# Performance work log

Hardware: AMD Instinct MI355X
Metric: run time of the kernel (lower is better)

Reference implementation:

```python
import jax, jax.numpy as jnp
import numpy as np
import math

B, C, H, W = 128, 128, 16, 16
E, NH, MEM, K = 128, 8, 8, 3
HD = E // NH            # head dim = 16
D = H * W * E // NH     # tot_head_dim = 4096
ATTN_MASK_B = 3.0
EPS = 1e-5


def conv_same(x, w, b):
    # x: (B, Cin, H, W), w: (Cout, Cin, K, K)  -- matches torch Conv2d with padding=K//2
    y = jax.lax.conv_general_dilated(x, w, (1, 1), 'SAME',
                                     dimension_numbers=('NCHW', 'OIHW', 'NCHW'))
    return y + b[None, :, None, None]


def setup_inputs() -> dict:
    key = jax.random.key(0)
    ks = jax.random.split(key, 12)
    s = 0.02
    return {
        'input':    jax.random.normal(ks[0], (B, C, H, W), jnp.float32),
        'h_cur':    jax.random.normal(ks[1], (B, E, H, W), jnp.float32),
        'c_cur':    jax.random.normal(ks[2], (B, E, H, W), jnp.float32),
        'concat_k': jax.random.normal(ks[3], (B, NH, MEM, D), jnp.float32),
        'concat_v': jax.random.normal(ks[4], (B, NH, MEM, D), jnp.float32),
        'attn_mask': jax.random.bernoulli(ks[5], 0.3, (B * NH, 1, MEM)),
        'main_w':   jax.random.normal(ks[6], (5 * E, C + E, K, K), jnp.float32) * s,
        'main_b':   jnp.zeros((5 * E,), jnp.float32),
        'proj_w':   jax.random.normal(ks[7], (3 * E, C, K, K), jnp.float32) * s,
        'proj_b':   jnp.zeros((3 * E,), jnp.float32),
        'out_w':    jax.random.normal(ks[8], (E, E, K, K), jnp.float32) * s,
        'out_b':    jnp.zeros((E,), jnp.float32),
        'norm_w':   jnp.ones((E, H, W), jnp.float32),
        'norm_b':   jnp.zeros((E, H, W), jnp.float32),
        'pos_w':    jax.random.normal(ks[9], (MEM, H * W * E), jnp.float32) * s,
        'pos_b':    jax.random.uniform(ks[10], (MEM, NH), jnp.float32, -0.1, 0.1),
    }


def reference(input, h_cur, c_cur, concat_k, concat_v, attn_mask,
              main_w, main_b, proj_w, proj_b, out_w, out_b,
              norm_w, norm_b, pos_w, pos_b):
    b = input.shape[0]
    BH = b * NH

    # ---- ConvLSTM gates (5 * embed_dim channels) ----
    combined = jnp.concatenate([input, h_cur], axis=1)           # (B, C+E, H, W)
    cc = conv_same(combined, main_w, main_b)                     # (B, 5E, H, W)
    cc_i, cc_f, cc_o, cc_g, cc_a = jnp.split(cc, 5, axis=1)
    i = jax.nn.sigmoid(cc_i)
    f = jax.nn.sigmoid(cc_f)
    o = jax.nn.sigmoid(cc_o)
    g = jnp.tanh(cc_g)
    a = jax.nn.sigmoid(cc_a)
    c_next = f * c_cur + i * g

    # ---- attention over rolling memory ----
    kqv = conv_same(input, proj_w, proj_b)                       # (B, 3E, H, W)
    kqv = kqv.reshape(BH, 3 * HD, H * W)                         # per-head groups of 3*HD channels
    k_new, q, v_new = jnp.split(kqv, 3, axis=1)                  # each (BH, HD, HW)
    flat = lambda x: x.reshape(BH, 1, D)                         # (BH, 1, tot_head_dim)
    q = flat(q) / math.sqrt(D)
    k_new, v_new = flat(k_new), flat(v_new)

    # slide memory: drop oldest slot, append new k/v
    k = jnp.concatenate([concat_k.reshape(BH, MEM, D)[:, 1:], k_new], axis=1)  # (BH, MEM, D)
    v = jnp.concatenate([concat_v.reshape(BH, MEM, D)[:, 1:], v_new], axis=1)

    # learned positional terms: pos_w added to keys, pos_b added to scores
    pw = pos_w.reshape(MEM, NH, D).transpose(1, 0, 2)            # (NH, MEM, D)
    k = (k.reshape(b, NH, MEM, D) + pw[None]).reshape(BH, MEM, D)
    pb = jnp.broadcast_to(pos_b.T[None], (b, NH, MEM)).reshape(BH, 1, MEM)

    # custom mask: -inf where masked, then last (newest) slot forced to +attn_mask_b bias
    mask_f = jnp.where(attn_mask, -jnp.inf, 0.0).astype(q.dtype)
    mask_f = mask_f.at[:, :, -1].set(ATTN_MASK_B)                # (BH, 1, MEM)

    scores = mask_f + jnp.einsum('bqd,bmd->bqm', q, k) + pb      # (BH, 1, MEM)
    attn_weights = jax.nn.softmax(scores, axis=-1)
    attn_out = jnp.einsum('bqm,bmd->bqd', attn_weights, v)       # (BH, 1, D)
    attn_out = attn_out.reshape(b, E, H, W)                      # (b,NH,HD,H,W)->(b,E,H,W)

    out = conv_same(attn_out, out_w, out_b) + input[:, :E]
    # LayerNorm over (E, H, W)
    mu = jnp.mean(out, axis=(1, 2, 3), keepdims=True)
    var = jnp.mean(jnp.square(out - mu), axis=(1, 2, 3), keepdims=True)
    out = (out - mu) * jax.lax.rsqrt(var + EPS) * norm_w[None] + norm_b[None]

    c_next = c_next + a * jnp.tanh(out)
    h_next = o * jnp.tanh(c_next)

    ret_k = k.reshape(b, NH, MEM, D)
    ret_v = v.reshape(b, NH, MEM, D)
    return h_next, c_next, ret_k, ret_v
```

## Files before the change

kernel.cpp:

```cpp
#include <hip/hip_runtime.h>
#include <hip/hip_bf16.h>

typedef __hip_bfloat16 bf16;
typedef __attribute__((ext_vector_type(8))) short bf16x8;
typedef __attribute__((ext_vector_type(4))) float f32x4;

__device__ __forceinline__ float b2f(bf16 x){ return __bfloat162float(x); }
__device__ __forceinline__ bf16  f2b(float x){ return __float2bfloat16(x); }
__device__ __forceinline__ float sigm(float x){ return 1.f/(1.f+__expf(-x)); }

__device__ __forceinline__ int sniff_bf16(const void* nw){
    return ((const unsigned short*)nw)[0] != 0;
}
__device__ __forceinline__ float ldf(const void* p, size_t i, int isb){
    return isb ? b2f(((const bf16*)p)[i]) : ((const float*)p)[i];
}
__device__ __forceinline__ void stf(void* p, size_t i, float v, int isb){
    if (isb) ((bf16*)p)[i] = f2b(v);
    else     ((float*)p)[i] = v;
}
__device__ __forceinline__ void ld8(const void* p, size_t i, int isb, float* a){
    if (isb){
        union{ uint4 u; bf16 h[8]; } x;
        x.u = *(const uint4*)((const bf16*)p + i);
        #pragma unroll
        for (int q=0;q<8;q++) a[q] = b2f(x.h[q]);
    } else {
        const float4* f4 = (const float4*)((const float*)p + i);
        float4 v0 = f4[0], v1 = f4[1];
        a[0]=v0.x;a[1]=v0.y;a[2]=v0.z;a[3]=v0.w;
        a[4]=v1.x;a[5]=v1.y;a[6]=v1.z;a[7]=v1.w;
    }
}
__device__ __forceinline__ void st8(void* p, size_t i, const float* a, int isb){
    if (isb){
        union{ uint4 u; bf16 h[8]; } o;
        #pragma unroll
        for (int q=0;q<8;q++) o.h[q] = f2b(a[q]);
        *(uint4*)((bf16*)p + i) = o.u;
    } else {
        float4* f4 = (float4*)((float*)p + i);
        f4[0] = make_float4(a[0],a[1],a[2],a[3]);
        f4[1] = make_float4(a[4],a[5],a[6],a[7]);
    }
}

#define H_OFF  0u
#define C_OFF  4194304u
#define RK_OFF 8388608u
#define RV_OFF 41943040u

__global__ void k_rearrange_mfma(const void* __restrict__ w, bf16* __restrict__ wrB,
                                 int nst, int NT, int mode,
                                 const void* __restrict__ nw)
{
    int isb = sniff_bf16(nw);
    int tid = blockIdx.x*256 + threadIdx.x;
    int total = nst*36*NT*64;
    if (tid >= total) return;
    int lane = tid & 63; int r = tid >> 6;
    int nt = r % NT; int kc = r / NT;
    int cb = kc & 3; int tp = (kc>>2) % 9; int s = kc / 36;
    int n = lane & 15, lg = lane >> 4;
    int oc;
    if (mode == 1){ int eb = nt/5, g = nt%5; oc = g*128 + eb*16 + n; }
    else if (mode == 2){ int h = nt/3, rr = nt%3; oc = h*48 + rr*16 + n; }
    else oc = nt*16 + n;
    int Cin = nst*128;
    int ci0 = s*128 + cb*32 + lg*8;
    size_t base = ((size_t)oc*Cin + ci0)*9 + tp;
    bf16* o = wrB + (size_t)tid*8;
    #pragma unroll
    for (int j=0;j<8;j++) o[j] = f2b(ldf(w, base + (size_t)j*9, isb));
}

__device__ __forceinline__ void stage_img(bf16* lds, const void* src, size_t base,
                                          int t, int isb)
{
    if (isb){
        const uint4* s4 = (const uint4*)((const bf16*)src + base);
        uint4* l4 = (uint4*)lds;
        for (int i=t; i<4096; i+=256) l4[i] = s4[i];
    } else {
        const float4* s4 = (const float4*)((const float*)src + base);
        for (int i=t; i<8192; i+=256){
            float4 v = s4[i];
            int j = i*4;
            lds[j]=f2b(v.x); lds[j+1]=f2b(v.y); lds[j+2]=f2b(v.z); lds[j+3]=f2b(v.w);
        }
    }
}

__global__ __launch_bounds__(256,2) void k_transpose(const void* __restrict__ src,
                                                     bf16* __restrict__ dst,
                                                     int nst, int sidx,
                                                     const void* __restrict__ nwp)
{
    int isb = nwp ? sniff_bf16(nwp) : 1;
    int b = blockIdx.x, t = threadIdx.x;
    __shared__ bf16 lds[32768];
    stage_img(lds, src, (size_t)b*32768, t, isb);
    __syncthreads();
    char* dimg = (char*)(dst + ((size_t)b*nst + sidx)*32768);
    int swz = (t & 7) << 4;
    for (int cb=0; cb<16; ++cb){
        union { uint4 u; bf16 h[8]; } o;
        #pragma unroll
        for (int q=0;q<8;q++) o.h[q] = lds[(cb*8+q)*256 + t];
        *(uint4*)(dimg + t*256 + ((cb*16) ^ swz)) = o.u;
    }
}

template<int NF, int NST>
__device__ __forceinline__ void conv_mfma(const bf16* __restrict__ xTimg,
                                          const bf16* __restrict__ wrB,
                                          int ntbase, int NT,
                                          bf16* lds, f32x4 (&acc)[4][NF])
{
    const int t = threadIdx.x;
    const int wid = t >> 6, lane = t & 63;
    const int lg = lane >> 4, x = lane & 15;
    union U { uint4 u; bf16x8 v; };

    for (int s=0; s<NST; ++s){
        __syncthreads();
        {
            const uint4* g4 = (const uint4*)(xTimg + (size_t)s*32768);
            uint4* l4 = (uint4*)lds;
            #pragma unroll
            for (int i=0;i<16;++i) l4[t + i*256] = g4[t + i*256];
        }
        __syncthreads();
        for (int tap=0; tap<9; ++tap){
            const int dy = tap/3 - 1, dx = tap%3 - 1;
            const int xx = x + dx;
            const bool xok = (unsigned)xx < 16u;
            const int xc = xx & 15;
            const int swz = (xc & 7) << 4;
            const char* ldsb = (const char*)lds;
            #pragma unroll
            for (int cb=0; cb<4; ++cb){
                U B[NF];
                const bf16* wb = wrB + ((size_t)(((s*9 + tap)*4 + cb)*NT + ntbase)*64 + lane)*8;
                #pragma unroll
                for (int nf=0; nf<NF; ++nf) B[nf].u = *(const uint4*)(wb + nf*512);
                const int cofs = (cb*64 + lg*16) ^ swz;
                #pragma unroll
                for (int mt=0; mt<4; ++mt){
                    const int yy = wid*4 + mt + dy;
                    if ((unsigned)yy < 16u){
                        U A;
                        A.u = *(const uint4*)(ldsb + (yy*16 + xc)*256 + cofs);
                        if (!xok) A.u = make_uint4(0u,0u,0u,0u);
                        #pragma unroll
                        for (int nf=0; nf<NF; ++nf)
                            acc[mt][nf] = __builtin_amdgcn_mfma_f32_16x16x32_bf16(
                                              A.v, B[nf].v, acc[mt][nf], 0, 0, 0);
                    }
                }
            }
        }
    }
}

template<int NF, int NFI>
__device__ __forceinline__ void epi_stage(float* lf, const f32x4 (&acc)[4][NF],
                                          int slotrow, int wid, int lg, int e)
{
    #pragma unroll
    for (int mt=0; mt<4; ++mt){
        int p = wid*64 + mt*16 + lg*4;
        #pragma unroll
        for (int r=0; r<4; ++r)
            lf[(slotrow + e)*257 + p + r] = acc[mt][NFI][r];
    }
}

__global__ __launch_bounds__(256,2) void k_main_mfma(
    const bf16* __restrict__ xT, const bf16* __restrict__ wrB,
    const void* __restrict__ bias, const void* __restrict__ ccur,
    bf16* __restrict__ wc, bf16* __restrict__ wo, bf16* __restrict__ wa,
    const void* __restrict__ nwp)
{
    int isb = sniff_bf16(nwp);
    int b = blockIdx.x, ocb = blockIdx.y, t = threadIdx.x;
    __shared__ bf16 lds[32768];
    f32x4 acc[4][5];
    const f32x4 z4 = {0.f,0.f,0.f,0.f};
    #pragma unroll
    for (int mt=0;mt<4;++mt)
        #pragma unroll
        for (int nf=0;nf<5;++nf) acc[mt][nf] = z4;

    conv_mfma<5,2>(xT + (size_t)b*65536, wrB, ocb*5, 40, lds, acc);

    __syncthreads();
    float* lf = (float*)lds;
    int wid = t>>6, lane = t&63, lg = lane>>4, e = lane&15;
    epi_stage<5,0>(lf, acc, 0,  wid, lg, e);
    epi_stage<5,1>(lf, acc, 16, wid, lg, e);
    epi_stage<5,3>(lf, acc, 32, wid, lg, e);
    __syncthreads();
    #pragma unroll
    for (int j=0;j<16;++j){
        int eg = ocb*16 + j;
        float gi = sigm (lf[(     j)*257 + t] + ldf(bias,       eg, isb));
        float gf = sigm (lf[(16 + j)*257 + t] + ldf(bias, 128 + eg, isb));
        float gg = tanhf(lf[(32 + j)*257 + t] + ldf(bias, 384 + eg, isb));
        size_t idx = ((size_t)b*128 + eg)*256 + t;
        float cp = ldf(ccur, idx, isb);
        wc[idx] = f2b(gf*cp + gi*gg);
    }
    __syncthreads();
    epi_stage<5,2>(lf, acc, 0,  wid, lg, e);
    epi_stage<5,4>(lf, acc, 16, wid, lg, e);
    __syncthreads();
    #pragma unroll
    for (int j=0;j<16;++j){
        int eg = ocb*16 + j;
        size_t idx = ((size_t)b*128 + eg)*256 + t;
        wo[idx] = f2b(sigm(lf[(     j)*257 + t] + ldf(bias, 256 + eg, isb)));
        wa[idx] = f2b(sigm(lf[(16 + j)*257 + t] + ldf(bias, 512 + eg, isb)));
    }
}

__global__ __launch_bounds__(256,2) void k_proj_mfma(
    const bf16* __restrict__ xT, const bf16* __restrict__ wrB,
    const void* __restrict__ bias, const void* __restrict__ pos_w,
    void* dout, bf16* __restrict__ wq, const void* __restrict__ nwp)
{
    int isb = sniff_bf16(nwp);
    int b = blockIdx.x, h = blockIdx.y, t = threadIdx.x;
    __shared__ bf16 lds[32768];
    f32x4 acc[4][3];
    const f32x4 z4 = {0.f,0.f,0.f,0.f};
    #pragma unroll
    for (int mt=0;mt<4;++mt)
        #pragma unroll
        for (int nf=0;nf<3;++nf) acc[mt][nf] = z4;

    conv_mfma<3,1>(xT + (size_t)b*65536, wrB, h*3, 24, lds, acc);

    __syncthreads();
    float* lf = (float*)lds;
    int wid = t>>6, lane = t&63, lg = lane>>4, e = lane&15;
    epi_stage<3,0>(lf, acc, 0,  wid, lg, e);
    epi_stage<3,1>(lf, acc, 16, wid, lg, e);
    epi_stage<3,2>(lf, acc, 32, wid, lg, e);
    __syncthreads();
    int bh = b*8 + h;
    #pragma unroll
    for (int j=0;j<16;++j){
        float kv = lf[(     j)*257 + t] + ldf(bias, h*48 +      j, isb);
        float qv = lf[(16 + j)*257 + t] + ldf(bias, h*48 + 16 + j, isb);
        float vv = lf[(32 + j)*257 + t] + ldf(bias, h*48 + 32 + j, isb);
        int d = j*256 + t;
        size_t kd = ((size_t)bh*8 + 7)*4096 + d;
        stf(dout, RK_OFF + kd, kv + ldf(pos_w, (size_t)7*32768 + h*4096 + d, isb), isb);
        stf(dout, RV_OFF + kd, vv, isb);
        wq[(size_t)bh*4096 + d] = f2b(qv * 0.015625f);
    }
}

__global__ __launch_bounds__(256,2) void k_out_mfma(
    const bf16* __restrict__ attnT, const bf16* __restrict__ wrB,
    const void* __restrict__ bias, const void* __restrict__ xin,
    bf16* __restrict__ wln, const void* __restrict__ nwp)
{
    int isb = sniff_bf16(nwp);
    int b = blockIdx.x, ocb = blockIdx.y, t = threadIdx.x;
    __shared__ bf16 lds[32768];
    f32x4 acc[4][2];
    const f32x4 z4 = {0.f,0.f,0.f,0.f};
    #pragma unroll
    for (int mt=0;mt<4;++mt)
        #pragma unroll
        for (int nf=0;nf<2;++nf) acc[mt][nf] = z4;

    conv_mfma<2,1>(attnT + (size_t)b*32768, wrB, ocb*2, 8, lds, acc);

    __syncthreads();
    float* lf = (float*)lds;
    int wid = t>>6, lane = t&63, lg = lane>>4, e = lane&15;
    epi_stage<2,0>(lf, acc, 0,  wid, lg, e);
    epi_stage<2,1>(lf, acc, 16, wid, lg, e);
    __syncthreads();
    #pragma unroll
    for (int o=0;o<32;++o){
        int oc = ocb*32 + o;
        size_t idx = ((size_t)b*128 + oc)*256 + t;
        wln[idx] = f2b(lf[o*257 + t] + ldf(bias, oc, isb) + ldf(xin, idx, isb));
    }
}

__global__ __launch_bounds__(256,2) void k_slide_attn(
    const void* __restrict__ ck, const void* __restrict__ cv,
    const void* __restrict__ pos_w, const bf16* __restrict__ wq,
    const int* __restrict__ mask, const void* __restrict__ pos_b,
    void* dout, bf16* __restrict__ attnT, const void* __restrict__ nwp)
{
    int isb = sniff_bf16(nwp);
    int bh = blockIdx.x, t = threadIdx.x;
    int b = bh >> 3, h = bh & 7;
    __shared__ float sbuf[4096];

    float qreg[2][8];
    #pragma unroll
    for (int j=0;j<2;j++){
        union{ uint4 u; bf16 hh[8]; } x;
        x.u = *(const uint4*)(wq + (size_t)bh*4096 + (size_t)(j*256+t)*8);
        #pragma unroll
        for (int q=0;q<8;q++) qreg[j][q] = b2f(x.hh[q]);
    }

    float part[8];
    #pragma unroll
    for (int m=0;m<8;m++) part[m]=0.f;
    for (int m=0;m<8;m++){
        #pragma unroll
        for (int j=0;j<2;j++){
            size_t d0 = (size_t)(j*256+t)*8;
            float a[8];
            if (m < 7){
                ld8(ck, ((size_t)bh*8 + m + 1)*4096 + d0, isb, a);
                float pv[8];
                ld8(pos_w, (size_t)m*32768 + (size_t)h*4096 + d0, isb, pv);
                #pragma unroll
                for (int q=0;q<8;q++) a[q] += pv[q];
                st8(dout, RK_OFF + ((size_t)bh*8 + m)*4096 + d0, a, isb);
            } else {
                ld8(dout, RK_OFF + ((size_t)bh*8 + 7)*4096 + d0, isb, a);
            }
            #pragma unroll
            for (int q=0;q<8;q++) part[m] = fmaf(qreg[j][q], a[q], part[m]);
        }
    }
    #pragma unroll
    for (int m=0;m<8;m++) sbuf[m*256 + t] = part[m];
    __syncthreads();
    for (int s=128; s>0; s>>=1){
        if (t < s){
            #pragma unroll
            for (int m=0;m<8;m++) sbuf[m*256 + t] += sbuf[m*256 + t + s];
        }
        __syncthreads();
    }
    float w[8]; float mx = -1e30f;
    #pragma unroll
    for (int m=0;m<8;m++){
        float mf = (m==7) ? 3.0f : (mask[bh*8+m] ? -INFINITY : 0.0f);
        w[m] = mf + sbuf[m*256] + ldf(pos_b, m*8 + h, isb);
        mx = fmaxf(mx, w[m]);
    }
    float ssum = 0.f;
    #pragma unroll
    for (int m=0;m<8;m++){ w[m] = __expf(w[m]-mx); ssum += w[m]; }
    float inv = 1.f/ssum;
    #pragma unroll
    for (int m=0;m<8;m++) w[m] *= inv;
    __syncthreads();

    float acc[2][8];
    #pragma unroll
    for (int j=0;j<2;j++)
        #pragma unroll
        for (int q=0;q<8;q++) acc[j][q]=0.f;
    for (int m=0;m<8;m++){
        #pragma unroll
        for (int j=0;j<2;j++){
            size_t d0 = (size_t)(j*256+t)*8;
            float a[8];
            if (m < 7){
                ld8(cv, ((size_t)bh*8 + m + 1)*4096 + d0, isb, a);
                st8(dout, RV_OFF + ((size_t)bh*8 + m)*4096 + d0, a, isb);
            } else {
                ld8(dout, RV_OFF + ((size_t)bh*8 + 7)*4096 + d0, isb, a);
            }
            #pragma unroll
            for (int q=0;q<8;q++) acc[j][q] = fmaf(w[m], a[q], acc[j][q]);
        }
    }
    #pragma unroll
    for (int j=0;j<2;j++){
        int chl = j*8 + (t>>5);
        int base = chl*256 + (t&31)*8;
        *(float4*)&sbuf[base    ] = make_float4(acc[j][0],acc[j][1],acc[j][2],acc[j][3]);
        *(float4*)&sbuf[base + 4] = make_float4(acc[j][4],acc[j][5],acc[j][6],acc[j][7]);
    }
    __syncthreads();
    int px = t, swz = (px & 7) << 4;
    union{ uint4 u; bf16 hh[8]; } o0, o1;
    #pragma unroll
    for (int jj=0;jj<8;jj++){
        o0.hh[jj] = f2b(sbuf[ jj     *256 + px]);
        o1.hh[jj] = f2b(sbuf[(jj+8)  *256 + px]);
    }
    char* dimg = (char*)(attnT + (size_t)b*32768);
    *(uint4*)(dimg + px*256 + ((h*32     ) ^ swz)) = o0.u;
    *(uint4*)(dimg + px*256 + ((h*32 + 16) ^ swz)) = o1.u;
}

__global__ __launch_bounds__(1024,1) void k_ln_stats(
    const bf16* __restrict__ wln, float2* __restrict__ stats)
{
    int b = blockIdx.x, t = threadIdx.x;
    float s = 0.f, s2 = 0.f;
    #pragma unroll
    for (int i=0;i<4;i++){
        union{ uint4 u; bf16 hh[8]; } x;
        x.u = *(const uint4*)(wln + (size_t)b*32768 + (size_t)(i*1024+t)*8);
        #pragma unroll
        for (int q=0;q<8;q++){ float v = b2f(x.hh[q]); s += v; s2 += v*v; }
    }
    #pragma unroll
    for (int off=32; off>0; off>>=1){
        s  += __shfl_down(s,  off);
        s2 += __shfl_down(s2, off);
    }
    __shared__ float r1[16], r2[16];
    int wv = t >> 6;
    if ((t & 63) == 0){ r1[wv] = s; r2[wv] = s2; }
    __syncthreads();
    if (t == 0){
        float a = 0.f, c = 0.f;
        #pragma unroll
        for (int k=0;k<16;k++){ a += r1[k]; c += r2[k]; }
        float mean = a * (1.f/32768.f);
        float var  = c * (1.f/32768.f) - mean*mean;
        stats[b] = make_float2(mean, rsqrtf(var + 1e-5f));
    }
}

__global__ __launch_bounds__(256,2) void k_ln_apply(
    const bf16* __restrict__ wln, const bf16* __restrict__ wc,
    const bf16* __restrict__ wo,  const bf16* __restrict__ wa,
    const void* __restrict__ nw,  const void* __restrict__ nb,
    const float2* __restrict__ stats, void* dout)
{
    int isb = sniff_bf16(nw);
    int b = blockIdx.x, sg = blockIdx.y, t = threadIdx.x;
    float2 mv = stats[b];
    float mean = mv.x, rs = mv.y;
    #pragma unroll
    for (int j=0;j<2;j++){
        size_t i  = (size_t)sg*4096 + (size_t)(j*256+t)*8;
        size_t gi = (size_t)b*32768 + i;
        union{ uint4 u; bf16 hh[8]; } xl, xc, xo, xa;
        xl.u = *(const uint4*)(wln + gi);
        xc.u = *(const uint4*)(wc  + gi);
        xo.u = *(const uint4*)(wo  + gi);
        xa.u = *(const uint4*)(wa  + gi);
        float nwv[8], nbv[8];
        ld8(nw, i, isb, nwv);
        ld8(nb, i, isb, nbv);
        float cts[8], hs[8];
        #pragma unroll
        for (int q=0;q<8;q++){
            float xln = (b2f(xl.hh[q]) - mean)*rs*nwv[q] + nbv[q];
            float ct  = b2f(xc.hh[q]) + b2f(xa.hh[q])*tanhf(xln);
            cts[q] = ct;
            hs[q]  = b2f(xo.hh[q])*tanhf(ct);
        }
        st8(dout, C_OFF + gi, cts, isb);
        st8(dout, H_OFF + gi, hs,  isb);
    }
}

extern "C" void kernel_launch(void* const* d_in, const int* in_sizes, int n_in,
                              void* d_out, int out_size, void* d_ws, size_t ws_size,
                              hipStream_t stream)
{
    const void* xin  = d_in[0];
    const void* hcur = d_in[1];
    const void* ccur = d_in[2];
    const void* ck   = d_in[3];
    const void* cv   = d_in[4];
    const int*  mask = (const int*) d_in[5];
    const void* mw   = d_in[6];
    const void* mb   = d_in[7];
    const void* pw   = d_in[8];
    const void* pb   = d_in[9];
    const void* ow   = d_in[10];
    const void* ob   = d_in[11];
    const void* nw   = d_in[12];
    const void* nb   = d_in[13];
    const void* posw = d_in[14];
    const void* posb = d_in[15];

    char* ws = (char*)d_ws;
    bf16* wrB_main = (bf16*)(ws + 0);
    bf16* wrB_proj = (bf16*)(ws + 2949120);
    bf16* wrB_out  = (bf16*)(ws + 3833856);
    bf16* wc  = (bf16*)(ws + 4128768);
    bf16* wo  = (bf16*)(ws + 12517376);
    bf16* wa  = (bf16*)(ws + 20905984);
    bf16* wq  = (bf16*)(ws + 29294592);
    bf16* wln = wq;
    float2* lnstats = (float2*)(ws + 37683200);

    bf16* xT    = (bf16*)d_out;
    bf16* attnT = xT + 4194304;

    k_rearrange_mfma<<<720,256,0,stream>>>(mw, wrB_main, 2, 40, 1, nw);
    k_rearrange_mfma<<<216,256,0,stream>>>(pw, wrB_proj, 1, 24, 2, nw);
    k_rearrange_mfma<<< 72,256,0,stream>>>(ow, wrB_out,  1,  8, 0, nw);

    k_transpose<<<128,256,0,stream>>>(xin,  xT, 2, 0, nw);
    k_transpose<<<128,256,0,stream>>>(hcur, xT, 2, 1, nw);

    k_main_mfma <<<dim3(128,8),256,0,stream>>>(xT, wrB_main, mb, ccur, wc, wo, wa, nw);
    k_proj_mfma <<<dim3(128,8),256,0,stream>>>(xT, wrB_proj, pb, posw, d_out, wq, nw);
    k_slide_attn<<<1024,       256,0,stream>>>(ck, cv, posw, wq, mask, posb, d_out, attnT, nw);
    k_out_mfma  <<<dim3(128,4),256,0,stream>>>(attnT, wrB_out, ob, xin, wln, nw);
    k_ln_stats  <<<128,       1024,0,stream>>>(wln, lnstats);
    k_ln_apply  <<<dim3(128,8),256,0,stream>>>(wln, wc, wo, wa, nw, nb, lnstats, d_out);
}
```

Measured before the change: 831.0 us.

## Halve conv LDS staging, fuse LN stats into out conv, merge transposes

The conv helper now stages each input image in two channel halves (128-byte rows), which shrinks the LDS footprint. Launch bounds are raised so more blocks fit per CU. LayerNorm statistics are accumulated in the output-conv epilogue with atomics, which removes the separate stats kernel but needs a memset to zero them first. The two transpose launches become one 2D grid, and the attention score reduction uses wave shuffles instead of an LDS tree. The trade-off is extra syncs per half-stage, a possible register-pressure increase, and non-deterministic atomic ordering in the stats.

```diff
diff --git a/kernel.cpp b/kernel.cpp
--- a/kernel.cpp
+++ b/kernel.cpp
@@ -91,22 +91,23 @@
     }
 }
 
-__global__ __launch_bounds__(256,2) void k_transpose(const void* __restrict__ src,
-                                                     bf16* __restrict__ dst,
-                                                     int nst, int sidx,
-                                                     const void* __restrict__ nwp)
-{
-    int isb = nwp ? sniff_bf16(nwp) : 1;
-    int b = blockIdx.x, t = threadIdx.x;
+__global__ __launch_bounds__(256,2) void k_transpose2(const void* __restrict__ x,
+                                                      const void* __restrict__ h,
+                                                      bf16* __restrict__ dst,
+                                                      const void* __restrict__ nwp)
+{
+    int isb = sniff_bf16(nwp);
+    int b = blockIdx.x, sidx = blockIdx.y, t = threadIdx.x;
+    const void* src = sidx ? h : x;
     __shared__ bf16 lds[32768];
     stage_img(lds, src, (size_t)b*32768, t, isb);
     __syncthreads();
-    char* dimg = (char*)(dst + ((size_t)b*nst + sidx)*32768);
+    char* dimg = (char*)(dst + ((size_t)b*2 + sidx)*32768);
     int swz = (t & 7) << 4;
     for (int cb=0; cb<16; ++cb){
-        union { uint4 u; bf16 h[8]; } o;
-        #pragma unroll
-        for (int q=0;q<8;q++) o.h[q] = lds[(cb*8+q)*256 + t];
+        union { uint4 u; bf16 hh[8]; } o;
+        #pragma unroll
+        for (int q=0;q<8;q++) o.hh[q] = lds[(cb*8+q)*256 + t];
         *(uint4*)(dimg + t*256 + ((cb*16) ^ swz)) = o.u;
     }
 }
@@ -120,42 +121,49 @@
     const int t = threadIdx.x;
     const int wid = t >> 6, lane = t & 63;
     const int lg = lane >> 4, x = lane & 15;
+    const int q8 = t & 7, pxg = t >> 3;
     union U { uint4 u; bf16x8 v; };
 
     for (int s=0; s<NST; ++s){
-        __syncthreads();
-        {
-            const uint4* g4 = (const uint4*)(xTimg + (size_t)s*32768);
-            uint4* l4 = (uint4*)lds;
-            #pragma unroll
-            for (int i=0;i<16;++i) l4[t + i*256] = g4[t + i*256];
-        }
-        __syncthreads();
-        for (int tap=0; tap<9; ++tap){
-            const int dy = tap/3 - 1, dx = tap%3 - 1;
-            const int xx = x + dx;
-            const bool xok = (unsigned)xx < 16u;
-            const int xc = xx & 15;
-            const int swz = (xc & 7) << 4;
-            const char* ldsb = (const char*)lds;
-            #pragma unroll
-            for (int cb=0; cb<4; ++cb){
-                U B[NF];
-                const bf16* wb = wrB + ((size_t)(((s*9 + tap)*4 + cb)*NT + ntbase)*64 + lane)*8;
+        const uint4* g4 = (const uint4*)(xTimg + (size_t)s*32768);
+        for (int hb=0; hb<2; ++hb){
+            __syncthreads();
+            {
+                uint4* l4 = (uint4*)lds;
                 #pragma unroll
-                for (int nf=0; nf<NF; ++nf) B[nf].u = *(const uint4*)(wb + nf*512);
-                const int cofs = (cb*64 + lg*16) ^ swz;
+                for (int p=0;p<8;++p){
+                    int px = pxg + p*32;
+                    l4[px*8 + q8] = g4[px*16 + hb*8 + q8];
+                }
+            }
+            __syncthreads();
+            for (int tap=0; tap<9; ++tap){
+                const int dy = tap/3 - 1, dx = tap%3 - 1;
+                const int xx = x + dx;
+                const bool xok = (unsigned)xx < 16u;
+                const int xc = xx & 15;
+                const int swz = (xc & 7) << 4;
+                const char* ldsb = (const char*)lds;
                 #pragma unroll
-                for (int mt=0; mt<4; ++mt){
-                    const int yy = wid*4 + mt + dy;
-                    if ((unsigned)yy < 16u){
-                        U A;
-                        A.u = *(const uint4*)(ldsb + (yy*16 + xc)*256 + cofs);
-                        if (!xok) A.u = make_uint4(0u,0u,0u,0u);
-                        #pragma unroll
-                        for (int nf=0; nf<NF; ++nf)
-                            acc[mt][nf] = __builtin_amdgcn_mfma_f32_16x16x32_bf16(
-                                              A.v, B[nf].v, acc[mt][nf], 0, 0, 0);
+                for (int ch=0; ch<2; ++ch){
+                    const int cb = hb*2 + ch;
+                    U B[NF];
+                    const bf16* wb = wrB + ((size_t)(((s*9 + tap)*4 + cb)*NT + ntbase)*64 + lane)*8;
+                    #pragma unroll
+                    for (int nf=0; nf<NF; ++nf) B[nf].u = *(const uint4*)(wb + nf*512);
+                    const int cofs = ((cb*64 + lg*16) ^ swz) & 127;
+                    #pragma unroll
+                    for (int mt=0; mt<4; ++mt){
+                        const int yy = wid*4 + mt + dy;
+                        if ((unsigned)yy < 16u){
+                            U A;
+                            A.u = *(const uint4*)(ldsb + (yy*16 + xc)*128 + cofs);
+                            if (!xok) A.u = make_uint4(0u,0u,0u,0u);
+                            #pragma unroll
+                            for (int nf=0; nf<NF; ++nf)
+                                acc[mt][nf] = __builtin_amdgcn_mfma_f32_16x16x32_bf16(
+                                                  A.v, B[nf].v, acc[mt][nf], 0, 0, 0);
+                        }
                     }
                 }
             }
@@ -176,7 +184,7 @@
     }
 }
 
-__global__ __launch_bounds__(256,2) void k_main_mfma(
+__global__ __launch_bounds__(256,3) void k_main_mfma(
     const bf16* __restrict__ xT, const bf16* __restrict__ wrB,
     const void* __restrict__ bias, const void* __restrict__ ccur,
     bf16* __restrict__ wc, bf16* __restrict__ wo, bf16* __restrict__ wa,
@@ -184,7 +192,8 @@
 {
     int isb = sniff_bf16(nwp);
     int b = blockIdx.x, ocb = blockIdx.y, t = threadIdx.x;
-    __shared__ bf16 lds[32768];
+    __shared__ __align__(16) float lf[12336];
+    bf16* lds = (bf16*)lf;
     f32x4 acc[4][5];
     const f32x4 z4 = {0.f,0.f,0.f,0.f};
     #pragma unroll
@@ -195,7 +204,6 @@
     conv_mfma<5,2>(xT + (size_t)b*65536, wrB, ocb*5, 40, lds, acc);
 
     __syncthreads();
-    float* lf = (float*)lds;
     int wid = t>>6, lane = t&63, lg = lane>>4, e = lane&15;
     epi_stage<5,0>(lf, acc, 0,  wid, lg, e);
     epi_stage<5,1>(lf, acc, 16, wid, lg, e);
@@ -224,14 +232,15 @@
     }
 }
 
-__global__ __launch_bounds__(256,2) void k_proj_mfma(
+__global__ __launch_bounds__(256,4) void k_proj_mfma(
     const bf16* __restrict__ xT, const bf16* __restrict__ wrB,
     const void* __restrict__ bias, const void* __restrict__ pos_w,
     void* dout, bf16* __restrict__ wq, const void* __restrict__ nwp)
 {
     int isb = sniff_bf16(nwp);
     int b = blockIdx.x, h = blockIdx.y, t = threadIdx.x;
-    __shared__ bf16 lds[32768];
+    __shared__ __align__(16) float lf[8224];
+    bf16* lds = (bf16*)lf;
     f32x4 acc[4][3];
     const f32x4 z4 = {0.f,0.f,0.f,0.f};
     #pragma unroll
@@ -242,34 +251,41 @@
     conv_mfma<3,1>(xT + (size_t)b*65536, wrB, h*3, 24, lds, acc);
 
     __syncthreads();
-    float* lf = (float*)lds;
     int wid = t>>6, lane = t&63, lg = lane>>4, e = lane&15;
+    int bh = b*8 + h;
     epi_stage<3,0>(lf, acc, 0,  wid, lg, e);
     epi_stage<3,1>(lf, acc, 16, wid, lg, e);
-    epi_stage<3,2>(lf, acc, 32, wid, lg, e);
-    __syncthreads();
-    int bh = b*8 + h;
+    __syncthreads();
     #pragma unroll
     for (int j=0;j<16;++j){
         float kv = lf[(     j)*257 + t] + ldf(bias, h*48 +      j, isb);
         float qv = lf[(16 + j)*257 + t] + ldf(bias, h*48 + 16 + j, isb);
-        float vv = lf[(32 + j)*257 + t] + ldf(bias, h*48 + 32 + j, isb);
         int d = j*256 + t;
         size_t kd = ((size_t)bh*8 + 7)*4096 + d;
         stf(dout, RK_OFF + kd, kv + ldf(pos_w, (size_t)7*32768 + h*4096 + d, isb), isb);
-        stf(dout, RV_OFF + kd, vv, isb);
         wq[(size_t)bh*4096 + d] = f2b(qv * 0.015625f);
     }
-}
-
-__global__ __launch_bounds__(256,2) void k_out_mfma(
+    __syncthreads();
+    epi_stage<3,2>(lf, acc, 0, wid, lg, e);
+    __syncthreads();
+    #pragma unroll
+    for (int j=0;j<16;++j){
+        float vv = lf[j*257 + t] + ldf(bias, h*48 + 32 + j, isb);
+        int d = j*256 + t;
+        stf(dout, RV_OFF + ((size_t)bh*8 + 7)*4096 + d, vv, isb);
+    }
+}
+
+__global__ __launch_bounds__(256,4) void k_out_mfma(
     const bf16* __restrict__ attnT, const bf16* __restrict__ wrB,
     const void* __restrict__ bias, const void* __restrict__ xin,
-    bf16* __restrict__ wln, const void* __restrict__ nwp)
+    bf16* __restrict__ wln, float* __restrict__ stats,
+    const void* __restrict__ nwp)
 {
     int isb = sniff_bf16(nwp);
     int b = blockIdx.x, ocb = blockIdx.y, t = threadIdx.x;
-    __shared__ bf16 lds[32768];
+    __shared__ __align__(16) float lf[8224];
+    bf16* lds = (bf16*)lf;
     f32x4 acc[4][2];
     const f32x4 z4 = {0.f,0.f,0.f,0.f};
     #pragma unroll
@@ -280,20 +296,38 @@
     conv_mfma<2,1>(attnT + (size_t)b*32768, wrB, ocb*2, 8, lds, acc);
 
     __syncthreads();
-    float* lf = (float*)lds;
     int wid = t>>6, lane = t&63, lg = lane>>4, e = lane&15;
     epi_stage<2,0>(lf, acc, 0,  wid, lg, e);
     epi_stage<2,1>(lf, acc, 16, wid, lg, e);
     __syncthreads();
+    float s = 0.f, s2 = 0.f;
     #pragma unroll
     for (int o=0;o<32;++o){
         int oc = ocb*32 + o;
         size_t idx = ((size_t)b*128 + oc)*256 + t;
-        wln[idx] = f2b(lf[o*257 + t] + ldf(bias, oc, isb) + ldf(xin, idx, isb));
-    }
-}
-
-__global__ __launch_bounds__(256,2) void k_slide_attn(
+        float val = lf[o*257 + t] + ldf(bias, oc, isb) + ldf(xin, idx, isb);
+        bf16 vb = f2b(val);
+        wln[idx] = vb;
+        float vq = b2f(vb);
+        s += vq; s2 += vq*vq;
+    }
+    __syncthreads();
+    #pragma unroll
+    for (int off=1; off<64; off<<=1){
+        s  += __shfl_xor(s,  off);
+        s2 += __shfl_xor(s2, off);
+    }
+    if (lane == 0){ lf[wid] = s; lf[4+wid] = s2; }
+    __syncthreads();
+    if (t == 0){
+        float a = lf[0]+lf[1]+lf[2]+lf[3];
+        float c = lf[4]+lf[5]+lf[6]+lf[7];
+        atomicAdd(&stats[2*b],   a);
+        atomicAdd(&stats[2*b+1], c);
+    }
+}
+
+__global__ __launch_bounds__(256,4) void k_slide_attn(
     const void* __restrict__ ck, const void* __restrict__ cv,
     const void* __restrict__ pos_w, const bf16* __restrict__ wq,
     const int* __restrict__ mask, const void* __restrict__ pos_b,
@@ -302,6 +336,7 @@
     int isb = sniff_bf16(nwp);
     int bh = blockIdx.x, t = threadIdx.x;
     int b = bh >> 3, h = bh & 7;
+    int wid = t >> 6, lane = t & 63;
     __shared__ float sbuf[4096];
 
     float qreg[2][8];
@@ -336,20 +371,21 @@
         }
     }
     #pragma unroll
-    for (int m=0;m<8;m++) sbuf[m*256 + t] = part[m];
-    __syncthreads();
-    for (int s=128; s>0; s>>=1){
-        if (t < s){
-            #pragma unroll
-            for (int m=0;m<8;m++) sbuf[m*256 + t] += sbuf[m*256 + t + s];
-        }
-        __syncthreads();
-    }
+    for (int off=1; off<64; off<<=1){
+        #pragma unroll
+        for (int m=0;m<8;m++) part[m] += __shfl_xor(part[m], off);
+    }
+    if (lane == 0){
+        #pragma unroll
+        for (int m=0;m<8;m++) sbuf[m*4 + wid] = part[m];
+    }
+    __syncthreads();
     float w[8]; float mx = -1e30f;
     #pragma unroll
     for (int m=0;m<8;m++){
         float mf = (m==7) ? 3.0f : (mask[bh*8+m] ? -INFINITY : 0.0f);
-        w[m] = mf + sbuf[m*256] + ldf(pos_b, m*8 + h, isb);
+        float sc = sbuf[m*4] + sbuf[m*4+1] + sbuf[m*4+2] + sbuf[m*4+3];
+        w[m] = mf + sc + ldf(pos_b, m*8 + h, isb);
         mx = fmaxf(mx, w[m]);
     }
     float ssum = 0.f;
@@ -400,47 +436,18 @@
     *(uint4*)(dimg + px*256 + ((h*32 + 16) ^ swz)) = o1.u;
 }
 
-__global__ __launch_bounds__(1024,1) void k_ln_stats(
-    const bf16* __restrict__ wln, float2* __restrict__ stats)
-{
-    int b = blockIdx.x, t = threadIdx.x;
-    float s = 0.f, s2 = 0.f;
-    #pragma unroll
-    for (int i=0;i<4;i++){
-        union{ uint4 u; bf16 hh[8]; } x;
-        x.u = *(const uint4*)(wln + (size_t)b*32768 + (size_t)(i*1024+t)*8);
-        #pragma unroll
-        for (int q=0;q<8;q++){ float v = b2f(x.hh[q]); s += v; s2 += v*v; }
-    }
-    #pragma unroll
-    for (int off=32; off>0; off>>=1){
-        s  += __shfl_down(s,  off);
-        s2 += __shfl_down(s2, off);
-    }
-    __shared__ float r1[16], r2[16];
-    int wv = t >> 6;
-    if ((t & 63) == 0){ r1[wv] = s; r2[wv] = s2; }
-    __syncthreads();
-    if (t == 0){
-        float a = 0.f, c = 0.f;
-        #pragma unroll
-        for (int k=0;k<16;k++){ a += r1[k]; c += r2[k]; }
-        float mean = a * (1.f/32768.f);
-        float var  = c * (1.f/32768.f) - mean*mean;
-        stats[b] = make_float2(mean, rsqrtf(var + 1e-5f));
-    }
-}
-
-__global__ __launch_bounds__(256,2) void k_ln_apply(
+__global__ __launch_bounds__(256,4) void k_ln_apply(
     const bf16* __restrict__ wln, const bf16* __restrict__ wc,
     const bf16* __restrict__ wo,  const bf16* __restrict__ wa,
     const void* __restrict__ nw,  const void* __restrict__ nb,
-    const float2* __restrict__ stats, void* dout)
+    const float* __restrict__ stats, void* dout)
 {
     int isb = sniff_bf16(nw);
     int b = blockIdx.x, sg = blockIdx.y, t = threadIdx.x;
-    float2 mv = stats[b];
-    float mean = mv.x, rs = mv.y;
+    float sum = stats[2*b], sumsq = stats[2*b+1];
+    float mean = sum * (1.f/32768.f);
+    float var  = sumsq * (1.f/32768.f) - mean*mean;
+    float rs   = rsqrtf(var + 1e-5f);
     #pragma unroll
     for (int j=0;j<2;j++){
         size_t i  = (size_t)sg*4096 + (size_t)(j*256+t)*8;
@@ -496,7 +503,7 @@
     bf16* wa  = (bf16*)(ws + 20905984);
     bf16* wq  = (bf16*)(ws + 29294592);
     bf16* wln = wq;
-    float2* lnstats = (float2*)(ws + 37683200);
+    float* lnstats = (float*)(ws + 37683200);
 
     bf16* xT    = (bf16*)d_out;
     bf16* attnT = xT + 4194304;
@@ -505,13 +512,12 @@
     k_rearrange_mfma<<<216,256,0,stream>>>(pw, wrB_proj, 1, 24, 2, nw);
     k_rearrange_mfma<<< 72,256,0,stream>>>(ow, wrB_out,  1,  8, 0, nw);
 
-    k_transpose<<<128,256,0,stream>>>(xin,  xT, 2, 0, nw);
-    k_transpose<<<128,256,0,stream>>>(hcur, xT, 2, 1, nw);
+    hipMemsetAsync(lnstats, 0, 1024, stream);
+    k_transpose2<<<dim3(128,2),256,0,stream>>>(xin, hcur, xT, nw);
 
     k_main_mfma <<<dim3(128,8),256,0,stream>>>(xT, wrB_main, mb, ccur, wc, wo, wa, nw);
     k_proj_mfma <<<dim3(128,8),256,0,stream>>>(xT, wrB_proj, pb, posw, d_out, wq, nw);
     k_slide_attn<<<1024,       256,0,stream>>>(ck, cv, posw, wq, mask, posb, d_out, attnT, nw);
-    k_out_mfma  <<<dim3(128,4),256,0,stream>>>(attnT, wrB_out, ob, xin, wln, nw);
-    k_ln_stats  <<<128,       1024,0,stream>>>(wln, lnstats);
+    k_out_mfma  <<<dim3(128,4),256,0,stream>>>(attnT, wrB_out, ob, xin, wln, lnstats, nw);
     k_ln_apply  <<<dim3(128,8),256,0,stream>>>(wln, wc, wo, wa, nw, nb, lnstats, d_out);
 }
```

Result: no change. 833.0 us (+0.2%).
